# Performance work log

Measured on AMD Instinct MI355X. Metric: run time of the kernel, lower is better.

## Reference

```python
import jax, jax.numpy as jnp
import numpy as np

DIM = 1024
FF = 4096
BATCH = 4
SEQ = 2048
EPS = 1e-5


def setup_inputs() -> dict:
    key = jax.random.key(0)
    ks = jax.random.split(key, 8)
    x = jax.random.normal(ks[0], (BATCH, SEQ, DIM), dtype=jnp.float32)
    # phazor init: exp(2j*pi*arange(dim)/dim) * |randn(dim)|
    ang = 2.0 * np.pi * jnp.arange(DIM, dtype=jnp.float32) / DIM
    mag = jnp.abs(jax.random.normal(ks[1], (DIM,), dtype=jnp.float32))
    phazor_re = mag * jnp.cos(ang)
    phazor_im = mag * jnp.sin(ang)
    last_re = jax.random.normal(ks[2], (DIM,), dtype=jnp.float32)
    last_im = jax.random.normal(ks[3], (DIM,), dtype=jnp.float32)
    w1 = jax.random.normal(ks[4], (FF, DIM), dtype=jnp.float32) * DIM ** -0.5
    b1 = jnp.zeros((FF,), dtype=jnp.float32)
    w2 = jax.random.normal(ks[5], (DIM, FF), dtype=jnp.float32) * FF ** -0.5
    b2 = jnp.zeros((DIM,), dtype=jnp.float32)
    return {
        'x': x,
        'ln1_w': jnp.ones((DIM,), jnp.float32), 'ln1_b': jnp.zeros((DIM,), jnp.float32),
        'ln2_w': jnp.ones((DIM,), jnp.float32), 'ln2_b': jnp.zeros((DIM,), jnp.float32),
        'sc_lin': jnp.ones((DIM,), jnp.float32),
        'phazor_re': phazor_re, 'phazor_im': phazor_im,
        'last_re': last_re, 'last_im': last_im,
        'w1': w1, 'b1': b1, 'w2': w2, 'b2': b2,
    }


def _layer_norm(x, w, b):
    mu = jnp.mean(x, axis=-1, keepdims=True)
    var = jnp.mean(jnp.square(x - mu), axis=-1, keepdims=True)
    return (x - mu) * jax.lax.rsqrt(var + EPS) * w + b


def _sconv(x, phazor_re, phazor_im, last_re, last_im):
    B, L, D = x.shape
    dtype = x.dtype
    xc = x.astype(jnp.complex64)
    p_raw = phazor_re + 1j * phazor_im
    # tanh(|p|) * exp(i*angle(p))
    p = (jnp.tanh(jnp.abs(p_raw)) * jnp.exp(1j * jnp.angle(p_raw))).astype(jnp.complex64)
    t = jnp.arange(L)[:, None]
    prog = jnp.power(p[None, :], t)            # [L, D] complex
    filt_fft = jnp.fft.fft(prog, n=2 * L, axis=0)   # [2L, D]
    x_fft = jnp.fft.fft(xc, n=2 * L, axis=1)        # [B, 2L, D]
    conv = jnp.fft.ifft(filt_fft[None] * x_fft, axis=1)[:, :L]  # [B, L, D]
    last = (last_re + 1j * last_im)[None, None, :]  # [1,1,D] broadcast over batch
    conv_with_past = conv + last * prog[None] * p[None, None]
    return conv_with_past.real.astype(dtype)


def reference(x, ln1_w, ln1_b, ln2_w, ln2_b, sc_lin,
              phazor_re, phazor_im, last_re, last_im,
              w1, b1, w2, b2):
    # SConv branch
    x_res = x
    h = _layer_norm(x, ln1_w, ln1_b)
    h = jax.nn.silu(h)
    h = _sconv(h, phazor_re, phazor_im, last_re, last_im)
    h = h * sc_lin
    x = h + x_res
    # FFN branch
    x_res = x
    h = _layer_norm(x, ln2_w, ln2_b)
    h = jax.nn.silu(jnp.einsum('bld,fd->blf', h, w1) + b1)
    h = jnp.einsum('blf,df->bld', h, w2) + b2
    return h + x_res
```

## Files before the change

kernel.cpp:

```cpp
#include <hip/hip_runtime.h>
#include <cmath>


#define DIMD 1024
#define FFD  4096
#define BATCH 4
#define SEQL 2048
#define MROWS (BATCH*SEQL)
#define EPSF 1e-5f
#define CHUNKS 32
#define CLEN (SEQL/CHUNKS)

typedef __attribute__((ext_vector_type(8))) _Float16 half8;
typedef __attribute__((ext_vector_type(4))) _Float16 half4;
typedef __attribute__((ext_vector_type(4))) float    floatx4;

#define H_OFF    0u
#define E_OFF    33554432u
#define SIN_OFF  34603008u
#define H2_OFF   35651584u
#define W1H_OFF  52428800u
#define W2H_OFF  60817408u
#define Y1_OFF   69206016u

__device__ __forceinline__ void load_lds16(const _Float16* g, _Float16* l) {
    __builtin_amdgcn_global_load_lds(
        (const __attribute__((address_space(1))) unsigned int*)g,
        (__attribute__((address_space(3))) unsigned int*)l,
        16, 0, 0);
}

__global__ __launch_bounds__(256)
void cast_f32_f16(const float* __restrict__ src, _Float16* __restrict__ dst) {
    int i = (blockIdx.x * 256 + threadIdx.x) * 4;
    float4 v = *(const float4*)(src + i);
    half4 o;
    o.x = (_Float16)v.x; o.y = (_Float16)v.y; o.z = (_Float16)v.z; o.w = (_Float16)v.w;
    *(half4*)(dst + i) = o;
}

__global__ __launch_bounds__(256)
void ln_kernel(const float* __restrict__ x, const float* __restrict__ w,
               const float* __restrict__ b, float* __restrict__ of,
               _Float16* __restrict__ oh, int mode) {
    const size_t row = blockIdx.x;
    const int tid = threadIdx.x;
    float4 v = *(const float4*)(x + row * DIMD + tid * 4);
    float s = (v.x + v.y) + (v.z + v.w);
    float q = (v.x * v.x + v.y * v.y) + (v.z * v.z + v.w * v.w);
    #pragma unroll
    for (int off = 32; off; off >>= 1) {
        s += __shfl_down(s, off, 64);
        q += __shfl_down(q, off, 64);
    }
    __shared__ float red[8];
    if (!(tid & 63)) { red[tid >> 6] = s; red[4 + (tid >> 6)] = q; }
    __syncthreads();
    s = (red[0] + red[1]) + (red[2] + red[3]);
    q = (red[4] + red[5]) + (red[6] + red[7]);
    const float mu = s * (1.f / DIMD);
    const float rs = rsqrtf(q * (1.f / DIMD) - mu * mu + EPSF);
    float4 wv = *(const float4*)(w + tid * 4);
    float4 bv = *(const float4*)(b + tid * 4);
    float o0 = (v.x - mu) * rs * wv.x + bv.x;
    float o1 = (v.y - mu) * rs * wv.y + bv.y;
    float o2 = (v.z - mu) * rs * wv.z + bv.z;
    float o3 = (v.w - mu) * rs * wv.w + bv.w;
    if (mode == 1) {
        o0 = o0 / (1.f + __expf(-o0));
        o1 = o1 / (1.f + __expf(-o1));
        o2 = o2 / (1.f + __expf(-o2));
        o3 = o3 / (1.f + __expf(-o3));
        float4 ov = {o0, o1, o2, o3};
        *(float4*)(of + row * DIMD + tid * 4) = ov;
    } else {
        half4 hv;
        hv.x = (_Float16)o0; hv.y = (_Float16)o1;
        hv.z = (_Float16)o2; hv.w = (_Float16)o3;
        *(half4*)(oh + row * DIMD + tid * 4) = hv;
    }
}

__device__ __forceinline__ void get_p(const float* pre, const float* pim, int d,
                                      float& pr, float& pi) {
    float re = pre[d], im = pim[d];
    float r = sqrtf(re * re + im * im);
    float t = tanhf(r) / fmaxf(r, 1e-30f);
    pr = re * t; pi = im * t;
}

__global__ __launch_bounds__(256)
void scan_partial(const float* __restrict__ h, const float* __restrict__ pre,
                  const float* __restrict__ pim, float2* __restrict__ e) {
    const int d = blockIdx.x * 256 + threadIdx.x;
    const int c = blockIdx.y;
    const int bb = blockIdx.z;
    float pr, pi; get_p(pre, pim, d, pr, pi);
    float sr = 0.f, si = 0.f;
    const float* hp = h + ((size_t)bb * SEQL + (size_t)c * CLEN) * DIMD + d;
    #pragma unroll 4
    for (int j = 0; j < CLEN; ++j) {
        float hv = hp[(size_t)j * DIMD];
        float nr = pr * sr - pi * si + hv;
        float ni = pr * si + pi * sr;
        sr = nr; si = ni;
    }
    e[((size_t)bb * CHUNKS + c) * DIMD + d] = make_float2(sr, si);
}

__global__ __launch_bounds__(256)
void scan_combine(const float2* __restrict__ e, const float* __restrict__ pre,
                  const float* __restrict__ pim, const float* __restrict__ lre,
                  const float* __restrict__ lim, float2* __restrict__ sv) {
    const int d = blockIdx.x * 256 + threadIdx.x;
    const int bb = blockIdx.y;
    float pr, pi; get_p(pre, pim, d, pr, pi);
    float qr = pr, qi = pi;
    #pragma unroll
    for (int s = 0; s < 6; ++s) {
        float nr = qr * qr - qi * qi;
        float ni = 2.f * qr * qi;
        qr = nr; qi = ni;
    }
    float sr = lre[d], si = lim[d];
    for (int c = 0; c < CHUNKS; ++c) {
        sv[((size_t)bb * CHUNKS + c) * DIMD + d] = make_float2(sr, si);
        float2 ec = e[((size_t)bb * CHUNKS + c) * DIMD + d];
        float nr = qr * sr - qi * si + ec.x;
        float ni = qr * si + qi * sr + ec.y;
        sr = nr; si = ni;
    }
}

__global__ __launch_bounds__(256)
void scan_final(const float* __restrict__ h, const float* __restrict__ x,
                const float* __restrict__ pre, const float* __restrict__ pim,
                const float* __restrict__ sc, const float2* __restrict__ sv,
                float* __restrict__ x2) {
    const int d = blockIdx.x * 256 + threadIdx.x;
    const int c = blockIdx.y;
    const int bb = blockIdx.z;
    float pr, pi; get_p(pre, pim, d, pr, pi);
    float2 s0 = sv[((size_t)bb * CHUNKS + c) * DIMD + d];
    float sr = s0.x, si = s0.y;
    const float scd = sc[d];
    const size_t base = ((size_t)bb * SEQL + (size_t)c * CLEN) * DIMD + d;
    #pragma unroll 4
    for (int j = 0; j < CLEN; ++j) {
        float hv = h[base + (size_t)j * DIMD];
        float nr = pr * sr - pi * si + hv;
        float ni = pr * si + pi * sr;
        sr = nr; si = ni;
        x2[base + (size_t)j * DIMD] = x[base + (size_t)j * DIMD] + scd * sr;
    }
}

#define BM 128
#define BN 128
#define BK 64

__global__ __launch_bounds__(256)
void gemm_bt(const _Float16* __restrict__ A, const _Float16* __restrict__ W,
             const float* __restrict__ bias, _Float16* __restrict__ out_h,
             const float* resid, float* out_f, int N, int K, int epi) {
    __shared__ _Float16 As[BM * BK];
    __shared__ _Float16 Bs[BN * BK];
    const int tid  = threadIdx.x;
    const int lane = tid & 63;
    const int wave = tid >> 6;
    const int wm = (wave >> 1) * 64;
    const int wn = (wave & 1) * 64;
    const size_t m0 = (size_t)blockIdx.y * BM;
    const size_t n0 = (size_t)blockIdx.x * BN;
    const int fr = lane & 15;
    const int quad = lane >> 4;

    const int srow = wave * 32 + (lane >> 3);
    const int ccp  = ((lane & 7) ^ (lane >> 3)) * 8;
    const _Float16* ag = A + (m0 + srow) * (size_t)K + ccp;
    const _Float16* wg = W + (n0 + srow) * (size_t)K + ccp;
    _Float16* asl = &As[(wave * 32) * BK];
    _Float16* bsl = &Bs[(wave * 32) * BK];

    floatx4 acc[4][4] = {};

    for (int k0 = 0; k0 < K; k0 += BK) {
        #pragma unroll
        for (int t = 0; t < 4; ++t) {
            load_lds16(ag + k0 + (size_t)(t * 8) * K, asl + t * 8 * BK);
            load_lds16(wg + k0 + (size_t)(t * 8) * K, bsl + t * 8 * BK);
        }
        __syncthreads();
        #pragma unroll
        for (int kk = 0; kk < BK; kk += 32) {
            half8 af[4], bf[4];
            #pragma unroll
            for (int i = 0; i < 4; ++i) {
                const int slot = (((kk >> 3) + quad) ^ (fr & 7)) * 8;
                af[i] = *(const half8*)(&As[(wm + i * 16 + fr) * BK + slot]);
                bf[i] = *(const half8*)(&Bs[(wn + i * 16 + fr) * BK + slot]);
            }
            #pragma unroll
            for (int i = 0; i < 4; ++i)
                #pragma unroll
                for (int j = 0; j < 4; ++j)
                    acc[i][j] = __builtin_amdgcn_mfma_f32_16x16x32_f16(
                        af[i], bf[j], acc[i][j], 0, 0, 0);
        }
        __syncthreads();
    }

    #pragma unroll
    for (int i = 0; i < 4; ++i) {
        #pragma unroll
        for (int j = 0; j < 4; ++j) {
            #pragma unroll
            for (int r = 0; r < 4; ++r) {
                const size_t gm = m0 + wm + i * 16 + quad * 4 + r;
                const size_t gn = n0 + wn + j * 16 + fr;
                float v = acc[i][j][r] + bias[gn];
                if (epi == 1) {
                    float sl = v / (1.f + __expf(-v));
                    out_h[gm * N + gn] = (_Float16)sl;
                } else {
                    out_f[gm * N + gn] = v + resid[gm * N + gn];
                }
            }
        }
    }
}

extern "C" void kernel_launch(void* const* d_in, const int* in_sizes, int n_in,
                              void* d_out, int out_size, void* d_ws, size_t ws_size,
                              hipStream_t stream) {
    const float* x    = (const float*)d_in[0];
    const float* ln1w = (const float*)d_in[1];
    const float* ln1b = (const float*)d_in[2];
    const float* ln2w = (const float*)d_in[3];
    const float* ln2b = (const float*)d_in[4];
    const float* sc   = (const float*)d_in[5];
    const float* pre  = (const float*)d_in[6];
    const float* pim  = (const float*)d_in[7];
    const float* lre  = (const float*)d_in[8];
    const float* lim  = (const float*)d_in[9];
    const float* w1   = (const float*)d_in[10];
    const float* b1   = (const float*)d_in[11];
    const float* w2   = (const float*)d_in[12];
    const float* b2   = (const float*)d_in[13];

    char* ws = (char*)d_ws;
    float*      h   = (float*)(ws + H_OFF);
    float2*     e   = (float2*)(ws + E_OFF);
    float2*     sv  = (float2*)(ws + SIN_OFF);
    _Float16*   h2  = (_Float16*)(ws + H2_OFF);
    _Float16*   w1h = (_Float16*)(ws + W1H_OFF);
    _Float16*   w2h = (_Float16*)(ws + W2H_OFF);
    _Float16*   y1  = (_Float16*)(ws + Y1_OFF);
    float*      x2  = (float*)d_out;
    float*      outp = (float*)d_out;

    cast_f32_f16<<<dim3(FFD * DIMD / 1024), 256, 0, stream>>>(w1, w1h);
    cast_f32_f16<<<dim3(FFD * DIMD / 1024), 256, 0, stream>>>(w2, w2h);
    ln_kernel<<<dim3(MROWS), 256, 0, stream>>>(x, ln1w, ln1b, h, nullptr, 1);
    scan_partial<<<dim3(DIMD / 256, CHUNKS, BATCH), 256, 0, stream>>>(h, pre, pim, e);
    scan_combine<<<dim3(DIMD / 256, BATCH), 256, 0, stream>>>(e, pre, pim, lre, lim, sv);
    scan_final<<<dim3(DIMD / 256, CHUNKS, BATCH), 256, 0, stream>>>(h, x, pre, pim, sc, sv, x2);
    ln_kernel<<<dim3(MROWS), 256, 0, stream>>>(x2, ln2w, ln2b, nullptr, h2, 2);
    gemm_bt<<<dim3(FFD / BN, MROWS / BM), 256, 0, stream>>>(
        h2, w1h, b1, y1, nullptr, nullptr, FFD, DIMD, 1);
    gemm_bt<<<dim3(DIMD / BN, MROWS / BM), 256, 0, stream>>>(
        y1, w2h, b2, nullptr, x2, outp, DIMD, FFD, 2);
}
```

Baseline: 382.4 us.

## Store SConv activations in fp16, vectorise scan kernels, merge casts, wave-per-row LayerNorm

The SiLU(LN1) activation is now stored in fp16 instead of fp32, halving traffic for the two scan passes. The scan kernels each process four channels per thread with vector loads and stores, and the chunk count doubles to 64 (combine uses p^32). The two weight casts merge into one launch, and LayerNorm uses one wave per row with no shared-memory sync. Storing the recurrence input in fp16 adds some rounding error, and the scan grids shrink to 256 blocks of 256 threads.

```diff
diff --git a/kernel.cpp b/kernel.cpp
--- a/kernel.cpp
+++ b/kernel.cpp
@@ -8,7 +8,7 @@
 #define SEQL 2048
 #define MROWS (BATCH*SEQL)
 #define EPSF 1e-5f
-#define CHUNKS 32
+#define CHUNKS 64
 #define CLEN (SEQL/CHUNKS)
 
 typedef __attribute__((ext_vector_type(8))) _Float16 half8;
@@ -16,12 +16,12 @@
 typedef __attribute__((ext_vector_type(4))) float    floatx4;
 
 #define H_OFF    0u
-#define E_OFF    33554432u
-#define SIN_OFF  34603008u
-#define H2_OFF   35651584u
-#define W1H_OFF  52428800u
-#define W2H_OFF  60817408u
-#define Y1_OFF   69206016u
+#define E_OFF    16777216u
+#define SIN_OFF  18874368u
+#define H2_OFF   20971520u
+#define W1H_OFF  37748736u
+#define W2H_OFF  46137344u
+#define Y1_OFF   54525952u
 
 __device__ __forceinline__ void load_lds16(const _Float16* g, _Float16* l) {
     __builtin_amdgcn_global_load_lds(
@@ -31,8 +31,12 @@
 }
 
 __global__ __launch_bounds__(256)
-void cast_f32_f16(const float* __restrict__ src, _Float16* __restrict__ dst) {
+void cast2_f32_f16(const float* __restrict__ w1, const float* __restrict__ w2,
+                   _Float16* __restrict__ o1, _Float16* __restrict__ o2) {
     int i = (blockIdx.x * 256 + threadIdx.x) * 4;
+    const float* src = w1;
+    _Float16* dst = o1;
+    if (i >= FFD * DIMD) { i -= FFD * DIMD; src = w2; dst = o2; }
     float4 v = *(const float4*)(src + i);
     half4 o;
     o.x = (_Float16)v.x; o.y = (_Float16)v.y; o.z = (_Float16)v.z; o.w = (_Float16)v.w;
@@ -41,43 +45,46 @@
 
 __global__ __launch_bounds__(256)
 void ln_kernel(const float* __restrict__ x, const float* __restrict__ w,
-               const float* __restrict__ b, float* __restrict__ of,
-               _Float16* __restrict__ oh, int mode) {
-    const size_t row = blockIdx.x;
-    const int tid = threadIdx.x;
-    float4 v = *(const float4*)(x + row * DIMD + tid * 4);
-    float s = (v.x + v.y) + (v.z + v.w);
-    float q = (v.x * v.x + v.y * v.y) + (v.z * v.z + v.w * v.w);
+               const float* __restrict__ b, _Float16* __restrict__ oh, int do_silu) {
+    const int wave = threadIdx.x >> 6;
+    const int lane = threadIdx.x & 63;
+    const size_t row = (size_t)blockIdx.x * 4 + wave;
+    const float* xp = x + row * DIMD + lane * 16;
+    float4 v[4];
+    float s = 0.f, q = 0.f;
+    #pragma unroll
+    for (int t = 0; t < 4; ++t) {
+        v[t] = *(const float4*)(xp + t * 4);
+        s += (v[t].x + v[t].y) + (v[t].z + v[t].w);
+        q += (v[t].x * v[t].x + v[t].y * v[t].y) + (v[t].z * v[t].z + v[t].w * v[t].w);
+    }
     #pragma unroll
     for (int off = 32; off; off >>= 1) {
         s += __shfl_down(s, off, 64);
         q += __shfl_down(q, off, 64);
     }
-    __shared__ float red[8];
-    if (!(tid & 63)) { red[tid >> 6] = s; red[4 + (tid >> 6)] = q; }
-    __syncthreads();
-    s = (red[0] + red[1]) + (red[2] + red[3]);
-    q = (red[4] + red[5]) + (red[6] + red[7]);
+    s = __shfl(s, 0, 64);
+    q = __shfl(q, 0, 64);
     const float mu = s * (1.f / DIMD);
     const float rs = rsqrtf(q * (1.f / DIMD) - mu * mu + EPSF);
-    float4 wv = *(const float4*)(w + tid * 4);
-    float4 bv = *(const float4*)(b + tid * 4);
-    float o0 = (v.x - mu) * rs * wv.x + bv.x;
-    float o1 = (v.y - mu) * rs * wv.y + bv.y;
-    float o2 = (v.z - mu) * rs * wv.z + bv.z;
-    float o3 = (v.w - mu) * rs * wv.w + bv.w;
-    if (mode == 1) {
-        o0 = o0 / (1.f + __expf(-o0));
-        o1 = o1 / (1.f + __expf(-o1));
-        o2 = o2 / (1.f + __expf(-o2));
-        o3 = o3 / (1.f + __expf(-o3));
-        float4 ov = {o0, o1, o2, o3};
-        *(float4*)(of + row * DIMD + tid * 4) = ov;
-    } else {
+    #pragma unroll
+    for (int t = 0; t < 4; ++t) {
+        float4 wv = *(const float4*)(w + lane * 16 + t * 4);
+        float4 bv = *(const float4*)(b + lane * 16 + t * 4);
+        float o0 = (v[t].x - mu) * rs * wv.x + bv.x;
+        float o1 = (v[t].y - mu) * rs * wv.y + bv.y;
+        float o2 = (v[t].z - mu) * rs * wv.z + bv.z;
+        float o3 = (v[t].w - mu) * rs * wv.w + bv.w;
+        if (do_silu) {
+            o0 = o0 / (1.f + __expf(-o0));
+            o1 = o1 / (1.f + __expf(-o1));
+            o2 = o2 / (1.f + __expf(-o2));
+            o3 = o3 / (1.f + __expf(-o3));
+        }
         half4 hv;
         hv.x = (_Float16)o0; hv.y = (_Float16)o1;
         hv.z = (_Float16)o2; hv.w = (_Float16)o3;
-        *(half4*)(oh + row * DIMD + tid * 4) = hv;
+        *(half4*)(oh + row * DIMD + lane * 16 + t * 4) = hv;
     }
 }
 
@@ -90,68 +97,95 @@
 }
 
 __global__ __launch_bounds__(256)
-void scan_partial(const float* __restrict__ h, const float* __restrict__ pre,
+void scan_partial(const _Float16* __restrict__ h, const float* __restrict__ pre,
                   const float* __restrict__ pim, float2* __restrict__ e) {
-    const int d = blockIdx.x * 256 + threadIdx.x;
-    const int c = blockIdx.y;
-    const int bb = blockIdx.z;
-    float pr, pi; get_p(pre, pim, d, pr, pi);
-    float sr = 0.f, si = 0.f;
-    const float* hp = h + ((size_t)bb * SEQL + (size_t)c * CLEN) * DIMD + d;
+    const int d0 = threadIdx.x * 4;
+    const int c = blockIdx.x;
+    const int bb = blockIdx.y;
+    float pr[4], pi[4], sr[4] = {}, si[4] = {};
+    #pragma unroll
+    for (int q = 0; q < 4; ++q) get_p(pre, pim, d0 + q, pr[q], pi[q]);
+    const _Float16* hp = h + ((size_t)bb * SEQL + (size_t)c * CLEN) * DIMD + d0;
     #pragma unroll 4
     for (int j = 0; j < CLEN; ++j) {
-        float hv = hp[(size_t)j * DIMD];
-        float nr = pr * sr - pi * si + hv;
-        float ni = pr * si + pi * sr;
-        sr = nr; si = ni;
-    }
-    e[((size_t)bb * CHUNKS + c) * DIMD + d] = make_float2(sr, si);
+        half4 hv = *(const half4*)(hp + (size_t)j * DIMD);
+        #pragma unroll
+        for (int q = 0; q < 4; ++q) {
+            float nr = pr[q] * sr[q] - pi[q] * si[q] + (float)hv[q];
+            float ni = pr[q] * si[q] + pi[q] * sr[q];
+            sr[q] = nr; si[q] = ni;
+        }
+    }
+    float2* ep = e + ((size_t)bb * CHUNKS + c) * DIMD + d0;
+    #pragma unroll
+    for (int q = 0; q < 4; ++q) ep[q] = make_float2(sr[q], si[q]);
 }
 
 __global__ __launch_bounds__(256)
 void scan_combine(const float2* __restrict__ e, const float* __restrict__ pre,
                   const float* __restrict__ pim, const float* __restrict__ lre,
                   const float* __restrict__ lim, float2* __restrict__ sv) {
-    const int d = blockIdx.x * 256 + threadIdx.x;
+    const int d0 = threadIdx.x * 4;
     const int bb = blockIdx.y;
-    float pr, pi; get_p(pre, pim, d, pr, pi);
-    float qr = pr, qi = pi;
-    #pragma unroll
-    for (int s = 0; s < 6; ++s) {
-        float nr = qr * qr - qi * qi;
-        float ni = 2.f * qr * qi;
-        qr = nr; qi = ni;
-    }
-    float sr = lre[d], si = lim[d];
+    float pr[4], pi[4], qr[4], qi[4], sr[4], si[4];
+    #pragma unroll
+    for (int q = 0; q < 4; ++q) {
+        get_p(pre, pim, d0 + q, pr[q], pi[q]);
+        qr[q] = pr[q]; qi[q] = pi[q];
+        #pragma unroll
+        for (int s = 0; s < 5; ++s) {
+            float nr = qr[q] * qr[q] - qi[q] * qi[q];
+            float ni = 2.f * qr[q] * qi[q];
+            qr[q] = nr; qi[q] = ni;
+        }
+        sr[q] = lre[d0 + q]; si[q] = lim[d0 + q];
+    }
     for (int c = 0; c < CHUNKS; ++c) {
-        sv[((size_t)bb * CHUNKS + c) * DIMD + d] = make_float2(sr, si);
-        float2 ec = e[((size_t)bb * CHUNKS + c) * DIMD + d];
-        float nr = qr * sr - qi * si + ec.x;
-        float ni = qr * si + qi * sr + ec.y;
-        sr = nr; si = ni;
-    }
-}
-
-__global__ __launch_bounds__(256)
-void scan_final(const float* __restrict__ h, const float* __restrict__ x,
+        const size_t base = ((size_t)bb * CHUNKS + c) * DIMD + d0;
+        #pragma unroll
+        for (int q = 0; q < 4; ++q) {
+            sv[base + q] = make_float2(sr[q], si[q]);
+            float2 ec = e[base + q];
+            float nr = qr[q] * sr[q] - qi[q] * si[q] + ec.x;
+            float ni = qr[q] * si[q] + qi[q] * sr[q] + ec.y;
+            sr[q] = nr; si[q] = ni;
+        }
+    }
+}
+
+__global__ __launch_bounds__(256)
+void scan_final(const _Float16* __restrict__ h, const float* __restrict__ x,
                 const float* __restrict__ pre, const float* __restrict__ pim,
                 const float* __restrict__ sc, const float2* __restrict__ sv,
                 float* __restrict__ x2) {
-    const int d = blockIdx.x * 256 + threadIdx.x;
-    const int c = blockIdx.y;
-    const int bb = blockIdx.z;
-    float pr, pi; get_p(pre, pim, d, pr, pi);
-    float2 s0 = sv[((size_t)bb * CHUNKS + c) * DIMD + d];
-    float sr = s0.x, si = s0.y;
-    const float scd = sc[d];
-    const size_t base = ((size_t)bb * SEQL + (size_t)c * CLEN) * DIMD + d;
+    const int d0 = threadIdx.x * 4;
+    const int c = blockIdx.x;
+    const int bb = blockIdx.y;
+    float pr[4], pi[4], sr[4], si[4];
+    #pragma unroll
+    for (int q = 0; q < 4; ++q) {
+        get_p(pre, pim, d0 + q, pr[q], pi[q]);
+        float2 s0 = sv[((size_t)bb * CHUNKS + c) * DIMD + d0 + q];
+        sr[q] = s0.x; si[q] = s0.y;
+    }
+    float4 scv = *(const float4*)(sc + d0);
+    const size_t base = ((size_t)bb * SEQL + (size_t)c * CLEN) * DIMD + d0;
     #pragma unroll 4
     for (int j = 0; j < CLEN; ++j) {
-        float hv = h[base + (size_t)j * DIMD];
-        float nr = pr * sr - pi * si + hv;
-        float ni = pr * si + pi * sr;
-        sr = nr; si = ni;
-        x2[base + (size_t)j * DIMD] = x[base + (size_t)j * DIMD] + scd * sr;
+        half4 hv = *(const half4*)(h + base + (size_t)j * DIMD);
+        float4 xv = *(const float4*)(x + base + (size_t)j * DIMD);
+        float4 ov;
+        #pragma unroll
+        for (int q = 0; q < 4; ++q) {
+            float nr = pr[q] * sr[q] - pi[q] * si[q] + (float)hv[q];
+            float ni = pr[q] * si[q] + pi[q] * sr[q];
+            sr[q] = nr; si[q] = ni;
+        }
+        ov.x = xv.x + scv.x * sr[0];
+        ov.y = xv.y + scv.y * sr[1];
+        ov.z = xv.z + scv.z * sr[2];
+        ov.w = xv.w + scv.w * sr[3];
+        *(float4*)(x2 + base + (size_t)j * DIMD) = ov;
     }
 }
 
@@ -249,7 +283,7 @@
     const float* b2   = (const float*)d_in[13];
 
     char* ws = (char*)d_ws;
-    float*      h   = (float*)(ws + H_OFF);
+    _Float16*   h   = (_Float16*)(ws + H_OFF);
     float2*     e   = (float2*)(ws + E_OFF);
     float2*     sv  = (float2*)(ws + SIN_OFF);
     _Float16*   h2  = (_Float16*)(ws + H2_OFF);
@@ -259,13 +293,12 @@
     float*      x2  = (float*)d_out;
     float*      outp = (float*)d_out;
 
-    cast_f32_f16<<<dim3(FFD * DIMD / 1024), 256, 0, stream>>>(w1, w1h);
-    cast_f32_f16<<<dim3(FFD * DIMD / 1024), 256, 0, stream>>>(w2, w2h);
-    ln_kernel<<<dim3(MROWS), 256, 0, stream>>>(x, ln1w, ln1b, h, nullptr, 1);
-    scan_partial<<<dim3(DIMD / 256, CHUNKS, BATCH), 256, 0, stream>>>(h, pre, pim, e);
-    scan_combine<<<dim3(DIMD / 256, BATCH), 256, 0, stream>>>(e, pre, pim, lre, lim, sv);
-    scan_final<<<dim3(DIMD / 256, CHUNKS, BATCH), 256, 0, stream>>>(h, x, pre, pim, sc, sv, x2);
-    ln_kernel<<<dim3(MROWS), 256, 0, stream>>>(x2, ln2w, ln2b, nullptr, h2, 2);
+    cast2_f32_f16<<<dim3(2 * FFD * DIMD / 1024), 256, 0, stream>>>(w1, w2, w1h, w2h);
+    ln_kernel<<<dim3(MROWS / 4), 256, 0, stream>>>(x, ln1w, ln1b, h, 1);
+    scan_partial<<<dim3(CHUNKS, BATCH), 256, 0, stream>>>(h, pre, pim, e);
+    scan_combine<<<dim3(1, BATCH), 256, 0, stream>>>(e, pre, pim, lre, lim, sv);
+    scan_final<<<dim3(CHUNKS, BATCH), 256, 0, stream>>>(h, x, pre, pim, sc, sv, x2);
+    ln_kernel<<<dim3(MROWS / 4), 256, 0, stream>>>(x2, ln2w, ln2b, h2, 0);
     gemm_bt<<<dim3(FFD / BN, MROWS / BM), 256, 0, stream>>>(
         h2, w1h, b1, y1, nullptr, nullptr, FFD, DIMD, 1);
     gemm_bt<<<dim3(DIMD / BN, MROWS / BM), 256, 0, stream>>>(
```

New measurement: 400.8 us. 4.8% more time.
